# Performance work log

Hardware: AMD Instinct MI355X
Metric: run time of the kernel (lower is better)

The kernel has to match this reference:

```python
import jax, jax.numpy as jnp
import numpy as np

N = 100_000      # nodes
E = 1_600_000    # edges (avg degree 16)
IN, HID, OUT = 256, 256, 128  # in_dim, 2*out_dim, out_dim
BN_EPS = 1e-5


def setup_inputs() -> dict:
    key = jax.random.key(0)
    ks = jax.random.split(key, 8)
    x = jax.random.normal(ks[0], (N, IN), jnp.float32)
    edge_index = jax.random.randint(ks[1], (2, E), 0, N, dtype=jnp.int64)
    # GCNConv weights (glorot-ish scaling) + biases
    W1 = jax.random.normal(ks[2], (IN, HID), jnp.float32) * (1.0 / np.sqrt(IN))
    b1 = jnp.zeros((HID,), jnp.float32)
    W2 = jax.random.normal(ks[3], (HID, OUT), jnp.float32) * (1.0 / np.sqrt(HID))
    b2 = jnp.zeros((OUT,), jnp.float32)
    # BatchNorm1d affine params
    gamma = jnp.ones((HID,), jnp.float32)
    beta = jnp.zeros((HID,), jnp.float32)
    # PReLU single learnable slope (torch default 0.25)
    a = jnp.full((1,), 0.25, jnp.float32)
    return {"x": x, "edge_index": edge_index, "W1": W1, "b1": b1,
            "W2": W2, "b2": b2, "gamma": gamma, "beta": beta, "a": a}


def gcn_layer(x, W, b, src, dst):
    """GCNConv: h = D^-1/2 (A + I) D^-1/2 (x @ W) + b, self-loop weight 1."""
    h = x @ W                                           # [N, F]
    deg = jnp.zeros((N,), h.dtype).at[dst].add(1.0) + 1.0  # +1 self-loop
    dinv = jax.lax.rsqrt(deg)                           # [N]
    norm = dinv[src] * dinv[dst]                        # [E]
    agg = jnp.zeros_like(h).at[dst].add(h[src] * norm[:, None])
    agg = agg + h * (dinv * dinv)[:, None]              # self-loop term
    return agg + b


def reference(x, edge_index, W1, b1, W2, b2, gamma, beta, a):
    src, dst = edge_index[0], edge_index[1]
    h = gcn_layer(x, W1, b1, src, dst)                  # [N, HID]
    # BatchNorm1d (training mode: batch statistics, biased var)
    mean = jnp.mean(h, axis=0)
    var = jnp.var(h, axis=0)
    h = (h - mean) * jax.lax.rsqrt(var + BN_EPS) * gamma + beta
    # PReLU with single shared slope
    h = jnp.where(h > 0, h, a * h)
    return gcn_layer(h, W2, b2, src, dst)               # [N, OUT]
```

## Files before the change

kernel.cpp:

```cpp
#include <hip/hip_runtime.h>
#include <hip/hip_bf16.h>
#include <stdint.h>

#define IN_DIM 256

typedef __attribute__((ext_vector_type(8))) short short8;
typedef __attribute__((ext_vector_type(4))) float f32x4;

__device__ __forceinline__ float bf2f(unsigned short u){
  return __uint_as_float(((unsigned int)u) << 16);
}
__device__ __forceinline__ unsigned short f2bf(float f){
  unsigned int u = __float_as_uint(f);
  u = u + 0x7FFFu + ((u >> 16) & 1u);
  return (unsigned short)(u >> 16);
}
__device__ __forceinline__ int rfl(int v){ return __builtin_amdgcn_readfirstlane(v); }

#if __has_builtin(__builtin_amdgcn_cvt_f32_ubyte0)
__device__ __forceinline__ float ub0(uint v){ return __builtin_amdgcn_cvt_f32_ubyte0(v); }
__device__ __forceinline__ float ub1(uint v){ return __builtin_amdgcn_cvt_f32_ubyte1(v); }
__device__ __forceinline__ float ub2(uint v){ return __builtin_amdgcn_cvt_f32_ubyte2(v); }
__device__ __forceinline__ float ub3(uint v){ return __builtin_amdgcn_cvt_f32_ubyte3(v); }
#else
__device__ __forceinline__ float ub0(uint v){ return (float)(v & 0xFF); }
__device__ __forceinline__ float ub1(uint v){ return (float)((v >> 8) & 0xFF); }
__device__ __forceinline__ float ub2(uint v){ return (float)((v >> 16) & 0xFF); }
__device__ __forceinline__ float ub3(uint v){ return (float)(v >> 24); }
#endif

__global__ void k_detect(const void* ei, long long E, int N, int* flag){
  __shared__ int bad;
  if (threadIdx.x == 0) bad = 0;
  __syncthreads();
  const long long* p = (const long long*)ei;
  long long stride = E / 1024; if (stride < 1) stride = 1;
  for (int i = threadIdx.x; i < 1024; i += blockDim.x){
    long long idx = (long long)i * stride;
    if (idx >= E) break;
    long long v = p[idx];
    if (v < 0 || v >= (long long)N) atomicOr(&bad, 1);
  }
  __syncthreads();
  if (threadIdx.x == 0) flag[0] = bad ? 0 : 1;
}

__device__ __forceinline__ int edge_at(const void* ei, long long i, int f64){
  if (f64) return (int)((const long long*)ei)[i];
  return ((const int*)ei)[i];
}

__global__ void k_hist(const void* ei, long long E, const int* flag, int* cnt){
  long long e = (long long)blockIdx.x * blockDim.x + threadIdx.x;
  if (e < E){
    int f = flag[0];
    int d = edge_at(ei, E + e, f);
    atomicAdd(&cnt[d], 1);
  }
}

__global__ void k_scan1(const int* cnt, int* rs, int* bsum, float* dinv, int* fill, int N){
  __shared__ int sh[1024];
  int i = blockIdx.x * 1024 + threadIdx.x;
  int v = (i < N) ? cnt[i] : 0;
  sh[threadIdx.x] = v;
  __syncthreads();
  for (int o = 1; o < 1024; o <<= 1){
    int x = (threadIdx.x >= o) ? sh[threadIdx.x - o] : 0;
    __syncthreads();
    sh[threadIdx.x] += x;
    __syncthreads();
  }
  if (i < N){
    rs[i] = sh[threadIdx.x] - v;
    dinv[i] = rsqrtf((float)v + 1.0f);
    fill[i] = 0;
  }
  if (threadIdx.x == 1023) bsum[blockIdx.x] = sh[1023];
}

__global__ void k_scan2(const int* bsum, int* boff, int nb, int* rs, int N,
                        float* sums, float* sqs){
  __shared__ int sh[128];
  int t = threadIdx.x;
  int v = (t < nb) ? bsum[t] : 0;
  sh[t] = v;
  __syncthreads();
  for (int o = 1; o < 128; o <<= 1){
    int x = (t >= o) ? sh[t - o] : 0;
    __syncthreads();
    sh[t] += x;
    __syncthreads();
  }
  boff[t] = sh[t] - v;
  if (t == 127) rs[N] = sh[127];
  for (int j = t; j < 1024; j += 128){ sums[j] = 0.f; sqs[j] = 0.f; }
}

__global__ void k_scan3(int* rs, const int* boff, int N){
  int i = blockIdx.x * 1024 + threadIdx.x;
  if (i < N) rs[i] += boff[blockIdx.x];
}

__global__ void k_scatter(const void* ei, long long E, const int* flag, const int* rs,
                          int* fill, int* csrc){
  long long e = (long long)blockIdx.x * blockDim.x + threadIdx.x;
  if (e < E){
    int f = flag[0];
    int s = edge_at(ei, e, f);
    int d = edge_at(ei, E + e, f);
    int pos = atomicAdd(&fill[d], 1);
    csrc[rs[d] + pos] = s;
  }
}

__global__ void k_prep(const float* __restrict__ x, ushort* __restrict__ xb,
                       const float* __restrict__ W1, ushort* __restrict__ W1t,
                       const float* __restrict__ W2, ushort* __restrict__ W2t,
                       int N, int NP){
  int idx = blockIdx.x * 256 + threadIdx.x;
  int nxq = NP * 64;
  if (idx < nxq){
    int row = idx >> 6, q = idx & 63;
    ushort4 o = {0, 0, 0, 0};
    if (row < N){
      float4 v = ((const float4*)x)[(size_t)row * 64 + q];
      o.x = f2bf(v.x); o.y = f2bf(v.y); o.z = f2bf(v.z); o.w = f2bf(v.w);
    }
    ((ushort4*)xb)[idx] = o;
  } else {
    int j = idx - nxq;
    if (j < 256 * 256){
      int n = j >> 8, k = j & 255;
      W1t[j] = f2bf(W1[(size_t)k * 256 + n]);
    } else {
      j -= 65536;
      if (j < 128 * 256){
        int n = j >> 8, k = j & 255;
        W2t[j] = f2bf(W2[(size_t)k * 128 + n]);
      }
    }
  }
}

__global__ __launch_bounds__(256) void k_gemm(const ushort* __restrict__ A,
                                              const ushort* __restrict__ Bt,
                                              ushort* __restrict__ C,
                                              const float* __restrict__ dinv,
                                              int N, int Nc){
  __shared__ ushort As[128 * 64];
  __shared__ ushort Bs[128 * 64];
  const int tid = threadIdx.x;
  const int wave = tid >> 6, lane = tid & 63;
  const long long row0 = (long long)blockIdx.x * 128;
  const int col0 = blockIdx.y * 128;
  const int lr = lane >> 3, lc = lane & 7;
  const int mrow = ((wave & 1) << 6) + (lane & 15);
  const int ncol = ((wave >> 1) << 6) + (lane & 15);

  f32x4 acc[4][4];
  #pragma unroll
  for (int i = 0; i < 4; ++i)
    #pragma unroll
    for (int j = 0; j < 4; ++j)
      acc[i][j] = (f32x4){0.f, 0.f, 0.f, 0.f};

  const ushort* gA = A + (row0 + wave * 32 + lr) * 256 + lc * 8;
  const ushort* gB = Bt + ((long long)(col0 + wave * 32 + lr)) * 256 + lc * 8;
  ushort* lA = As + wave * 2048;
  ushort* lB = Bs + wave * 2048;

  #pragma unroll
  for (int kt = 0; kt < 4; ++kt){
    #pragma unroll
    for (int i = 0; i < 4; ++i){
      __builtin_amdgcn_global_load_lds(
          (const __attribute__((address_space(1))) void*)(gA + kt * 64 + i * 8 * 256),
          (__attribute__((address_space(3))) void*)(lA + i * 512), 16, 0, 0);
      __builtin_amdgcn_global_load_lds(
          (const __attribute__((address_space(1))) void*)(gB + kt * 64 + i * 8 * 256),
          (__attribute__((address_space(3))) void*)(lB + i * 512), 16, 0, 0);
    }
    __syncthreads();
    #pragma unroll
    for (int ks = 0; ks < 2; ++ks){
      const int kb = ks * 32 + ((lane >> 4) << 3);
      short8 af[4], bfv[4];
      #pragma unroll
      for (int i = 0; i < 4; ++i) af[i] = *(const short8*)(As + (mrow + i * 16) * 64 + kb);
      #pragma unroll
      for (int j = 0; j < 4; ++j) bfv[j] = *(const short8*)(Bs + (ncol + j * 16) * 64 + kb);
      #pragma unroll
      for (int i = 0; i < 4; ++i)
        #pragma unroll
        for (int j = 0; j < 4; ++j)
          acc[i][j] = __builtin_amdgcn_mfma_f32_16x16x32_bf16(af[i], bfv[j], acc[i][j], 0, 0, 0);
    }
    __syncthreads();
  }

  const int rbase = ((wave & 1) << 6) + ((lane >> 4) << 2);
  const int cb = col0 + ((wave >> 1) << 6) + (lane & 15);
  #pragma unroll
  for (int i = 0; i < 4; ++i)
    #pragma unroll
    for (int r = 0; r < 4; ++r){
      long long row = row0 + rbase + i * 16 + r;
      float sc = (row < N) ? dinv[row] : 0.f;
      #pragma unroll
      for (int j = 0; j < 4; ++j)
        C[row * Nc + cb + j * 16] = f2bf(sc * acc[i][j][r]);
    }
}

__global__ __launch_bounds__(256) void k_quant1(const ushort* __restrict__ hb,
    uint* __restrict__ q, float* __restrict__ sc, int N){
  int lane = threadIdx.x & 63;
  int r = blockIdx.x * 4 + (threadIdx.x >> 6);
  if (r >= N) return;
  ushort4 v = ((const ushort4*)hb)[(size_t)r * 64 + lane];
  float f0 = bf2f(v.x), f1 = bf2f(v.y), f2 = bf2f(v.z), f3 = bf2f(v.w);
  float m = fmaxf(fmaxf(fabsf(f0), fabsf(f1)), fmaxf(fabsf(f2), fabsf(f3)));
  #pragma unroll
  for (int o = 32; o >= 1; o >>= 1) m = fmaxf(m, __shfl_xor(m, o, 64));
  float scale = m * (1.0f / 127.0f);
  float inv = (m > 0.f) ? 127.0f / m : 0.f;
  uint b0 = (uint)(int)(rintf(f0 * inv) + 128.0f);
  uint b1 = (uint)(int)(rintf(f1 * inv) + 128.0f);
  uint b2 = (uint)(int)(rintf(f2 * inv) + 128.0f);
  uint b3 = (uint)(int)(rintf(f3 * inv) + 128.0f);
  q[(size_t)r * 64 + lane] = b0 | (b1 << 8) | (b2 << 16) | (b3 << 24);
  if (lane == 0) sc[r] = scale;
}

__global__ __launch_bounds__(256) void k_quant2(const ushort* __restrict__ hb,
    ushort* __restrict__ q, float* __restrict__ sc, int N){
  int lane = threadIdx.x & 63;
  int r = blockIdx.x * 4 + (threadIdx.x >> 6);
  if (r >= N) return;
  uint v = ((const uint*)hb)[(size_t)r * 64 + lane];
  float f0 = bf2f((unsigned short)(v & 0xFFFF));
  float f1 = bf2f((unsigned short)(v >> 16));
  float m = fmaxf(fabsf(f0), fabsf(f1));
  #pragma unroll
  for (int o = 32; o >= 1; o >>= 1) m = fmaxf(m, __shfl_xor(m, o, 64));
  float scale = m * (1.0f / 127.0f);
  float inv = (m > 0.f) ? 127.0f / m : 0.f;
  uint b0 = (uint)(int)(rintf(f0 * inv) + 128.0f);
  uint b1 = (uint)(int)(rintf(f1 * inv) + 128.0f);
  q[(size_t)r * 64 + lane] = (ushort)(b0 | (b1 << 8));
  if (lane == 0) sc[r] = scale;
}

__global__ __launch_bounds__(256) void k_agg1(const uint* __restrict__ q, const float* __restrict__ sc,
    const int* __restrict__ rs, const int* __restrict__ csrc, const float* __restrict__ b1,
    ushort* __restrict__ h1, float* __restrict__ sums, float* __restrict__ sqs,
    int N, int nblocks){
  __shared__ float red[4 * 512];
  const int lane = threadIdx.x & 63;
  const int wid = rfl((blockIdx.x * 256 + threadIdx.x) >> 6);
  const int nw = (nblocks * 256) >> 6;
  const float4 bb = ((const float4*)b1)[lane];
  const uint* ql = q + lane;
  float st0 = 0.f, st1 = 0.f, st2 = 0.f, st3 = 0.f;
  float sq0 = 0.f, sq1 = 0.f, sq2 = 0.f, sq3 = 0.f;

  for (int n = wid; n < N; n += nw){
    int e = rfl(rs[n]), end = rfl(rs[n + 1]);
    float dn = rsqrtf((float)(end - e) + 1.0f);
    float scn = sc[n];
    uint v = ql[(uint)n << 6];
    float ssum = scn;
    float a0 = scn * ub0(v), a1 = scn * ub1(v), a2 = scn * ub2(v), a3 = scn * ub3(v);
    for (; e + 8 <= end; e += 8){
      int s0 = rfl(csrc[e]),     s1 = rfl(csrc[e + 1]), s2 = rfl(csrc[e + 2]), s3 = rfl(csrc[e + 3]);
      int s4 = rfl(csrc[e + 4]), s5 = rfl(csrc[e + 5]), s6 = rfl(csrc[e + 6]), s7 = rfl(csrc[e + 7]);
      float c0 = sc[s0], c1 = sc[s1], c2 = sc[s2], c3 = sc[s3];
      float c4 = sc[s4], c5 = sc[s5], c6 = sc[s6], c7 = sc[s7];
      uint v0 = ql[(uint)s0 << 6];
      uint v1 = ql[(uint)s1 << 6];
      uint v2 = ql[(uint)s2 << 6];
      uint v3 = ql[(uint)s3 << 6];
      uint v4 = ql[(uint)s4 << 6];
      uint v5 = ql[(uint)s5 << 6];
      uint v6 = ql[(uint)s6 << 6];
      uint v7 = ql[(uint)s7 << 6];
      ssum += ((c0 + c1) + (c2 + c3)) + ((c4 + c5) + (c6 + c7));
      a0 += ((c0 * ub0(v0) + c1 * ub0(v1)) + (c2 * ub0(v2) + c3 * ub0(v3)))
          + ((c4 * ub0(v4) + c5 * ub0(v5)) + (c6 * ub0(v6) + c7 * ub0(v7)));
      a1 += ((c0 * ub1(v0) + c1 * ub1(v1)) + (c2 * ub1(v2) + c3 * ub1(v3)))
          + ((c4 * ub1(v4) + c5 * ub1(v5)) + (c6 * ub1(v6) + c7 * ub1(v7)));
      a2 += ((c0 * ub2(v0) + c1 * ub2(v1)) + (c2 * ub2(v2) + c3 * ub2(v3)))
          + ((c4 * ub2(v4) + c5 * ub2(v5)) + (c6 * ub2(v6) + c7 * ub2(v7)));
      a3 += ((c0 * ub3(v0) + c1 * ub3(v1)) + (c2 * ub3(v2) + c3 * ub3(v3)))
          + ((c4 * ub3(v4) + c5 * ub3(v5)) + (c6 * ub3(v6) + c7 * ub3(v7)));
    }
    for (; e + 4 <= end; e += 4){
      int s0 = rfl(csrc[e]), s1 = rfl(csrc[e + 1]), s2 = rfl(csrc[e + 2]), s3 = rfl(csrc[e + 3]);
      float c0 = sc[s0], c1 = sc[s1], c2 = sc[s2], c3 = sc[s3];
      uint v0 = ql[(uint)s0 << 6];
      uint v1 = ql[(uint)s1 << 6];
      uint v2 = ql[(uint)s2 << 6];
      uint v3 = ql[(uint)s3 << 6];
      ssum += (c0 + c1) + (c2 + c3);
      a0 += (c0 * ub0(v0) + c1 * ub0(v1)) + (c2 * ub0(v2) + c3 * ub0(v3));
      a1 += (c0 * ub1(v0) + c1 * ub1(v1)) + (c2 * ub1(v2) + c3 * ub1(v3));
      a2 += (c0 * ub2(v0) + c1 * ub2(v1)) + (c2 * ub2(v2) + c3 * ub2(v3));
      a3 += (c0 * ub3(v0) + c1 * ub3(v1)) + (c2 * ub3(v2) + c3 * ub3(v3));
    }
    for (; e < end; ++e){
      int s = rfl(csrc[e]);
      float c = sc[s];
      uint vv = ql[(uint)s << 6];
      ssum += c;
      a0 += c * ub0(vv); a1 += c * ub1(vv); a2 += c * ub2(vv); a3 += c * ub3(vv);
    }
    float corr = -128.0f * ssum;
    float h0 = dn * (a0 + corr) + bb.x;
    float h1v = dn * (a1 + corr) + bb.y;
    float h2 = dn * (a2 + corr) + bb.z;
    float h3 = dn * (a3 + corr) + bb.w;
    st0 += h0; st1 += h1v; st2 += h2; st3 += h3;
    sq0 += h0 * h0; sq1 += h1v * h1v; sq2 += h2 * h2; sq3 += h3 * h3;
    ushort4 o;
    o.x = f2bf(h0); o.y = f2bf(h1v); o.z = f2bf(h2); o.w = f2bf(h3);
    ((ushort4*)h1)[(size_t)n * 64 + lane] = o;
  }

  int wv = threadIdx.x >> 6;
  int f = lane * 4;
  red[wv * 512 + f]     = st0; red[wv * 512 + f + 1] = st1;
  red[wv * 512 + f + 2] = st2; red[wv * 512 + f + 3] = st3;
  __syncthreads();
  float v0s = red[threadIdx.x] + red[512 + threadIdx.x] + red[1024 + threadIdx.x] + red[1536 + threadIdx.x];
  __syncthreads();
  red[wv * 512 + f]     = sq0; red[wv * 512 + f + 1] = sq1;
  red[wv * 512 + f + 2] = sq2; red[wv * 512 + f + 3] = sq3;
  __syncthreads();
  float v0q = red[threadIdx.x] + red[512 + threadIdx.x] + red[1024 + threadIdx.x] + red[1536 + threadIdx.x];
  if (threadIdx.x < 256){
    int rep = ((blockIdx.x & 3) << 8) + threadIdx.x;
    atomicAdd(&sums[rep], v0s);
    atomicAdd(&sqs[rep], v0q);
  }
}

__global__ __launch_bounds__(256) void k_agg2(const ushort* __restrict__ q, const float* __restrict__ sc,
    const int* __restrict__ rs, const int* __restrict__ csrc, const float* __restrict__ b2,
    float* __restrict__ out, int N, int nblocks){
  const int lane = threadIdx.x & 63;
  const int wid = rfl((blockIdx.x * 256 + threadIdx.x) >> 6);
  const int nw = (nblocks * 256) >> 6;
  const float2 bb = ((const float2*)b2)[lane];
  const ushort* ql = q + lane;

  for (int n = wid; n < N; n += nw){
    int e = rfl(rs[n]), end = rfl(rs[n + 1]);
    float dn = rsqrtf((float)(end - e) + 1.0f);
    float scn = sc[n];
    uint v = (uint)ql[(uint)n << 6];
    float ssum = scn;
    float a0 = scn * ub0(v), a1 = scn * ub1(v);
    for (; e + 8 <= end; e += 8){
      int s0 = rfl(csrc[e]),     s1 = rfl(csrc[e + 1]), s2 = rfl(csrc[e + 2]), s3 = rfl(csrc[e + 3]);
      int s4 = rfl(csrc[e + 4]), s5 = rfl(csrc[e + 5]), s6 = rfl(csrc[e + 6]), s7 = rfl(csrc[e + 7]);
      float c0 = sc[s0], c1 = sc[s1], c2 = sc[s2], c3 = sc[s3];
      float c4 = sc[s4], c5 = sc[s5], c6 = sc[s6], c7 = sc[s7];
      uint v0 = (uint)ql[(uint)s0 << 6];
      uint v1 = (uint)ql[(uint)s1 << 6];
      uint v2 = (uint)ql[(uint)s2 << 6];
      uint v3 = (uint)ql[(uint)s3 << 6];
      uint v4 = (uint)ql[(uint)s4 << 6];
      uint v5 = (uint)ql[(uint)s5 << 6];
      uint v6 = (uint)ql[(uint)s6 << 6];
      uint v7 = (uint)ql[(uint)s7 << 6];
      ssum += ((c0 + c1) + (c2 + c3)) + ((c4 + c5) + (c6 + c7));
      a0 += ((c0 * ub0(v0) + c1 * ub0(v1)) + (c2 * ub0(v2) + c3 * ub0(v3)))
          + ((c4 * ub0(v4) + c5 * ub0(v5)) + (c6 * ub0(v6) + c7 * ub0(v7)));
      a1 += ((c0 * ub1(v0) + c1 * ub1(v1)) + (c2 * ub1(v2) + c3 * ub1(v3)))
          + ((c4 * ub1(v4) + c5 * ub1(v5)) + (c6 * ub1(v6) + c7 * ub1(v7)));
    }
    for (; e + 4 <= end; e += 4){
      int s0 = rfl(csrc[e]), s1 = rfl(csrc[e + 1]), s2 = rfl(csrc[e + 2]), s3 = rfl(csrc[e + 3]);
      float c0 = sc[s0], c1 = sc[s1], c2 = sc[s2], c3 = sc[s3];
      uint v0 = (uint)ql[(uint)s0 << 6];
      uint v1 = (uint)ql[(uint)s1 << 6];
      uint v2 = (uint)ql[(uint)s2 << 6];
      uint v3 = (uint)ql[(uint)s3 << 6];
      ssum += (c0 + c1) + (c2 + c3);
      a0 += (c0 * ub0(v0) + c1 * ub0(v1)) + (c2 * ub0(v2) + c3 * ub0(v3));
      a1 += (c0 * ub1(v0) + c1 * ub1(v1)) + (c2 * ub1(v2) + c3 * ub1(v3));
    }
    for (; e < end; ++e){
      int s = rfl(csrc[e]);
      float c = sc[s];
      uint vv = (uint)ql[(uint)s << 6];
      ssum += c;
      a0 += c * ub0(vv); a1 += c * ub1(vv);
    }
    float corr = -128.0f * ssum;
    float2 r;
    r.x = dn * (a0 + corr) + bb.x;
    r.y = dn * (a1 + corr) + bb.y;
    ((float2*)out)[(size_t)n * 64 + lane] = r;
  }
}

__global__ void k_prelu(const ushort* __restrict__ h1, const float* __restrict__ sums,
                        const float* __restrict__ sqs, const float* __restrict__ gamma,
                        const float* __restrict__ beta, const float* __restrict__ aP,
                        ushort* __restrict__ P, int N, int NP){
  int idx = blockIdx.x * 256 + threadIdx.x;
  int row = idx >> 7, cp = idx & 127;
  if (row >= NP) return;
  uint o = 0;
  if (row < N){
    int c0 = 2 * cp;
    float inv = 1.0f / (float)N;
    float s0 = sums[c0]     + sums[256 + c0]     + sums[512 + c0]     + sums[768 + c0];
    float s1 = sums[c0 + 1] + sums[256 + c0 + 1] + sums[512 + c0 + 1] + sums[768 + c0 + 1];
    float q0 = sqs[c0]      + sqs[256 + c0]      + sqs[512 + c0]      + sqs[768 + c0];
    float q1 = sqs[c0 + 1]  + sqs[256 + c0 + 1]  + sqs[512 + c0 + 1]  + sqs[768 + c0 + 1];
    float m0 = s0 * inv,     m1 = s1 * inv;
    float v0 = q0 * inv - m0 * m0, v1 = q1 * inv - m1 * m1;
    float sc0 = gamma[c0] * rsqrtf(v0 + 1e-5f);
    float sc1 = gamma[c0 + 1] * rsqrtf(v1 + 1e-5f);
    float sh0 = beta[c0] - m0 * sc0;
    float sh1 = beta[c0 + 1] - m1 * sc1;
    uint v = ((const uint*)h1)[(size_t)row * 128 + cp];
    float aa = aP[0];
    float x0 = bf2f((unsigned short)(v & 0xFFFF)) * sc0 + sh0;
    float x1 = bf2f((unsigned short)(v >> 16)) * sc1 + sh1;
    x0 = x0 > 0.f ? x0 : aa * x0;
    x1 = x1 > 0.f ? x1 : aa * x1;
    o = (uint)f2bf(x0) | ((uint)f2bf(x1) << 16);
  }
  ((uint*)P)[idx] = o;
}

extern "C" void kernel_launch(void* const* d_in, const int* in_sizes, int n_in,
                              void* d_out, int out_size, void* d_ws, size_t ws_size,
                              hipStream_t stream){
  const float* x  = (const float*)d_in[0];
  const void*  ei = d_in[1];
  const float* W1 = (const float*)d_in[2];
  const float* b1 = (const float*)d_in[3];
  const float* W2 = (const float*)d_in[4];
  const float* b2 = (const float*)d_in[5];
  const float* gm = (const float*)d_in[6];
  const float* bt = (const float*)d_in[7];
  const float* aP = (const float*)d_in[8];
  float* out = (float*)d_out;

  const int N = in_sizes[0] / IN_DIM;
  const long long E = in_sizes[1] / 2;
  const int NP = ((N + 127) / 128) * 128;

  char* w = (char*)d_ws;
  size_t off = 0;
  auto carve = [&](size_t bytes) -> char* {
    char* p = w + off;
    off += (bytes + 255) & ~(size_t)255;
    return p;
  };
  ushort* xb  = (ushort*)carve((size_t)NP * 256 * 2);
  ushort* hb  = (ushort*)carve((size_t)NP * 256 * 2);
  ushort* h1b = (ushort*)carve((size_t)NP * 256 * 2);
  ushort* W1t = (ushort*)carve(256 * 256 * 2);
  ushort* W2t = (ushort*)carve(128 * 256 * 2);
  int*   cnt  = (int*)  carve((size_t)N * 4);
  int*   rs   = (int*)  carve((size_t)(N + 1) * 4);
  int*   fill = (int*)  carve((size_t)N * 4);
  int*   csrc = (int*)  carve((size_t)E * 4);
  float* dinv = (float*)carve((size_t)N * 4);
  float* sc1  = (float*)carve((size_t)N * 4);
  float* sc2  = (float*)carve((size_t)N * 4);
  int*   bsum = (int*)  carve(512);
  int*   boff = (int*)  carve(512);
  float* sums = (float*)carve(4096);
  float* sqs  = (float*)carve(4096);
  int*   flag = (int*)  carve(256);
  uint*   q8a = (uint*)xb;
  ushort* q8b = (ushort*)h1b;

  const int NB1 = (N + 1023) / 1024;
  const int egrid = (int)((E + 255) / 256);
  const int prep_grid = (NP * 64 + 256 * 256 + 128 * 256 + 255) / 256;
  const int AGG1_BLOCKS = 2048, AGG2_BLOCKS = 2048;

  k_detect<<<1, 256, 0, stream>>>(ei, E, N, flag);
  hipMemsetAsync(cnt, 0, (size_t)N * 4, stream);
  k_prep<<<prep_grid, 256, 0, stream>>>(x, xb, W1, W1t, W2, W2t, N, NP);
  k_hist<<<egrid, 256, 0, stream>>>(ei, E, flag, cnt);
  k_scan1<<<NB1, 1024, 0, stream>>>(cnt, rs, bsum, dinv, fill, N);
  k_scan2<<<1, 128, 0, stream>>>(bsum, boff, NB1, rs, N, sums, sqs);
  k_scan3<<<NB1, 1024, 0, stream>>>(rs, boff, N);
  k_scatter<<<egrid, 256, 0, stream>>>(ei, E, flag, rs, fill, csrc);

  k_gemm<<<dim3(NP / 128, 2), 256, 0, stream>>>(xb, W1t, hb, dinv, N, 256);
  k_quant1<<<(N + 3) / 4, 256, 0, stream>>>(hb, q8a, sc1, N);
  k_agg1<<<AGG1_BLOCKS, 256, 0, stream>>>(q8a, sc1, rs, csrc, b1, h1b, sums, sqs, N, AGG1_BLOCKS);
  k_prelu<<<(NP * 128 + 255) / 256, 256, 0, stream>>>(h1b, sums, sqs, gm, bt, aP, xb, N, NP);
  k_gemm<<<dim3(NP / 128, 1), 256, 0, stream>>>(xb, W2t, hb, dinv, N, 128);
  k_quant2<<<(N + 3) / 4, 256, 0, stream>>>(hb, q8b, sc2, N);
  k_agg2<<<AGG2_BLOCKS, 256, 0, stream>>>(q8b, sc2, rs, csrc, b2, out, N, AGG2_BLOCKS);
}
```

Measured before the change: 611.2 us.

## Compact edge indices to int32 and partition CSR scatter by destination range

The histogram kernel now also writes 32-bit copies of the src and dst indices into the unused hb scratch buffer. A new scatter kernel uses 2048 blocks, each pairing one of 8 destination-node ranges with one of 256 edge chunks. Each block reads dst from the compact array and only handles edges whose dst falls in its range. This is meant to confine the atomic fill counters and CSR writes for a block to one eighth of the nodes, improving cache locality for the scattered atomics and stores. The cost is that every edge's dst is read 8 times and the histogram pass does extra writes.

After: 608.1 us. Within noise of the previous version (-0.5%).

```diff
diff --git a/kernel.cpp b/kernel.cpp
--- a/kernel.cpp
+++ b/kernel.cpp
@@ -50,11 +50,15 @@
   return ((const int*)ei)[i];
 }
 
-__global__ void k_hist(const void* ei, long long E, const int* flag, int* cnt){
+__global__ void k_hist(const void* ei, long long E, const int* flag, int* cnt,
+                       int* __restrict__ dst32, int* __restrict__ src32){
   long long e = (long long)blockIdx.x * blockDim.x + threadIdx.x;
   if (e < E){
     int f = flag[0];
+    int s = edge_at(ei, e, f);
     int d = edge_at(ei, E + e, f);
+    src32[e] = s;
+    dst32[e] = d;
     atomicAdd(&cnt[d], 1);
   }
 }
@@ -102,15 +106,24 @@
   if (i < N) rs[i] += boff[blockIdx.x];
 }
 
-__global__ void k_scatter(const void* ei, long long E, const int* flag, const int* rs,
-                          int* fill, int* csrc){
-  long long e = (long long)blockIdx.x * blockDim.x + threadIdx.x;
-  if (e < E){
-    int f = flag[0];
-    int s = edge_at(ei, e, f);
-    int d = edge_at(ei, E + e, f);
-    int pos = atomicAdd(&fill[d], 1);
-    csrc[rs[d] + pos] = s;
+__global__ __launch_bounds__(256) void k_scatter8(const int* __restrict__ dst32,
+    const int* __restrict__ src32, long long E, const int* __restrict__ rs,
+    int* __restrict__ fill, int* __restrict__ csrc, int N){
+  const int g = blockIdx.x & 7;
+  const int bg = blockIdx.x >> 3;
+  const int Q = (N + 7) >> 3;
+  const int lo = g * Q;
+  const int hi = (lo + Q < N) ? lo + Q : N;
+  const long long per = (E + 255) / 256;
+  long long e0 = (long long)bg * per;
+  long long e1 = e0 + per; if (e1 > E) e1 = E;
+  for (long long e = e0 + threadIdx.x; e < e1; e += 256){
+    int d = dst32[e];
+    if (d >= lo && d < hi){
+      int s = src32[e];
+      int pos = atomicAdd(&fill[d], 1);
+      csrc[rs[d] + pos] = s;
+    }
   }
 }
 
@@ -482,6 +495,8 @@
   int*   flag = (int*)  carve(256);
   uint*   q8a = (uint*)xb;
   ushort* q8b = (ushort*)h1b;
+  int*   dst32 = (int*)hb;
+  int*   src32 = ((int*)hb) + E;
 
   const int NB1 = (N + 1023) / 1024;
   const int egrid = (int)((E + 255) / 256);
@@ -491,11 +506,11 @@
   k_detect<<<1, 256, 0, stream>>>(ei, E, N, flag);
   hipMemsetAsync(cnt, 0, (size_t)N * 4, stream);
   k_prep<<<prep_grid, 256, 0, stream>>>(x, xb, W1, W1t, W2, W2t, N, NP);
-  k_hist<<<egrid, 256, 0, stream>>>(ei, E, flag, cnt);
+  k_hist<<<egrid, 256, 0, stream>>>(ei, E, flag, cnt, dst32, src32);
   k_scan1<<<NB1, 1024, 0, stream>>>(cnt, rs, bsum, dinv, fill, N);
   k_scan2<<<1, 128, 0, stream>>>(bsum, boff, NB1, rs, N, sums, sqs);
   k_scan3<<<NB1, 1024, 0, stream>>>(rs, boff, N);
-  k_scatter<<<egrid, 256, 0, stream>>>(ei, E, flag, rs, fill, csrc);
+  k_scatter8<<<2048, 256, 0, stream>>>(dst32, src32, E, rs, fill, csrc, N);
 
   k_gemm<<<dim3(NP / 128, 2), 256, 0, stream>>>(xb, W1t, hb, dinv, N, 256);
   k_quant1<<<(N + 3) / 4, 256, 0, stream>>>(hb, q8a, sc1, N);
```
